# Kernel tuning notes

Measured on AMD Instinct MI355X. Metric: run time of the kernel, lower is better.

Reference implementation:

```python
import jax, jax.numpy as jnp
import numpy as np

B, N, F, C = 8, 1024, 2048, 4
H = F // 2

def setup_inputs() -> dict:
    key = jax.random.key(0)
    k0, k1, k2 = jax.random.split(key, 3)
    vectors = jax.random.normal(k0, (B, N, F), jnp.float32)  # pooled per-mask backbone features
    W1 = jax.random.normal(k1, (H, 2 * F), jnp.float32) * np.float32(1.0 / np.sqrt(2 * F))
    b1 = jnp.zeros((H,), jnp.float32)
    W2 = jax.random.normal(k2, (C, H), jnp.float32) * np.float32(1.0 / np.sqrt(H))
    b2 = jnp.zeros((C,), jnp.float32)
    return {"vectors": vectors, "W1": W1, "b1": b1, "W2": W2, "b2": b2}

def reference(vectors, W1, b1, W2, b2):
    # Original: for each pair (i, j): sigmoid(L2(L1(cat(v_i, v_j)))).
    # There is NO nonlinearity between the two Linears, so the composition is
    # exactly linear in (v_i, v_j):
    #   logits[b,i,j] = W2 @ (W1a v_i + W1b v_j + b1) + b2
    # which factors into two per-node projections + a pairwise broadcast add,
    # avoiding the [B,N,N,H] intermediate.
    f = vectors.shape[-1]
    W1a, W1b = W1[:, :f], W1[:, f:]
    p1 = jnp.einsum('bnh,ch->bnc', jnp.einsum('bnf,hf->bnh', vectors, W1a), W2)  # [B,N,C]
    p2 = jnp.einsum('bnh,ch->bnc', jnp.einsum('bnf,hf->bnh', vectors, W1b), W2)  # [B,N,C]
    const = W2 @ b1 + b2  # [C]
    logits = p1[:, :, None, :] + p2[:, None, :, :] + const  # [B, i, j, C]
    # torch code stacks j along dim=2 and i along dim=3 -> connections[b,c,j,i]
    connections = jax.nn.sigmoid(logits).transpose(0, 3, 2, 1)  # [B, C, N_j, N_i]
    return vectors, connections
```

## Files before the change

kernel.cpp:

```cpp
#include <hip/hip_runtime.h>
#include <hip/hip_bf16.h>

#define BB 8
#define NN 1024
#define FF 2048
#define CC 4
#define HH 1024
#define ROWS (BB * NN)
#define MELEMS (8 * FF)

typedef float f4 __attribute__((ext_vector_type(4)));

__device__ __forceinline__ float sigmoidf_fast(float x) {
    return __builtin_amdgcn_rcpf(1.0f + __expf(-x));
}

__device__ __forceinline__ float butterfly8(float a[8], int lane) {
    #pragma unroll
    for (int i = 0; i < 4; ++i) {
        float send = (lane & 1) ? a[i] : a[i + 4];
        float got = __shfl_xor(send, 1, 64);
        a[i] = ((lane & 1) ? a[i + 4] : a[i]) + got;
    }
    #pragma unroll
    for (int i = 0; i < 2; ++i) {
        float send = (lane & 2) ? a[i] : a[i + 2];
        float got = __shfl_xor(send, 2, 64);
        a[i] = ((lane & 2) ? a[i + 2] : a[i]) + got;
    }
    {
        float send = (lane & 4) ? a[0] : a[1];
        float got = __shfl_xor(send, 4, 64);
        a[0] = ((lane & 4) ? a[1] : a[0]) + got;
    }
    a[0] += __shfl_xor(a[0], 8, 64);
    a[0] += __shfl_xor(a[0], 16, 64);
    a[0] += __shfl_xor(a[0], 32, 64);
    return a[0];
}

__global__ __launch_bounds__(256) void k_fold(const float* __restrict__ W1,
                                              const float* __restrict__ W2,
                                              const float* __restrict__ b1,
                                              const float* __restrict__ b2,
                                              float* __restrict__ Mpart,
                                              float* __restrict__ cst,
                                              int hper, int nchunks) {
    int chunk = blockIdx.y;
    if (chunk == nchunks) {
        if (blockIdx.x != 0) return;
        int t = threadIdx.x;
        int c = t >> 6, lane = t & 63;
        float s = 0.f;
        for (int h = lane; h < HH; h += 64) s += W2[c * HH + h] * b1[h];
        #pragma unroll
        for (int off = 32; off; off >>= 1) s += __shfl_down(s, off);
        if (lane == 0) cst[c] = s + b2[c];
        return;
    }
    int k4 = (blockIdx.x * 256 + threadIdx.x) << 2;
    int half = k4 >> 11;
    int f = k4 & (FF - 1);
    int h0 = chunk * hper;
    f4 a0 = {0.f, 0.f, 0.f, 0.f}, a1 = a0, a2 = a0, a3 = a0;
    const float* base = W1 + (size_t)h0 * (2 * FF) + k4;
    #pragma unroll 16
    for (int i = 0; i < hper; ++i) {
        f4 wv = *(const f4*)(base + (size_t)i * (2 * FF));
        int h = h0 + i;
        float s0 = W2[0 * HH + h], s1 = W2[1 * HH + h];
        float s2 = W2[2 * HH + h], s3 = W2[3 * HH + h];
        a0 += wv * s0;
        a1 += wv * s1;
        a2 += wv * s2;
        a3 += wv * s3;
    }
    float* mp = Mpart + (size_t)chunk * MELEMS + (size_t)(half * 4) * FF + f;
    *(f4*)(mp + 0 * FF) = a0;
    *(f4*)(mp + 1 * FF) = a1;
    *(f4*)(mp + 2 * FF) = a2;
    *(f4*)(mp + 3 * FF) = a3;
}

__global__ __launch_bounds__(256) void k_reduce(const float* __restrict__ Mpart,
                                                float* __restrict__ M,
                                                int nchunks) {
    int idx4 = blockIdx.x * 256 + threadIdx.x;
    f4 s = {0.f, 0.f, 0.f, 0.f};
    const f4* mp = (const f4*)Mpart;
    #pragma unroll 16
    for (int p = 0; p < nchunks; ++p) s += mp[(size_t)p * (MELEMS / 4) + idx4];
    ((f4*)M)[idx4] = s;
}

__global__ __launch_bounds__(256) void k_pcompute(const float* __restrict__ v,
                                                  const float* __restrict__ M,
                                                  float* __restrict__ outv,
                                                  float* __restrict__ P1,
                                                  float* __restrict__ P2) {
    int t = threadIdx.x;
    int lane = t & 63, wvi = t >> 6;
    int f0 = t * 8;
    float w[8][8];
    #pragma unroll
    for (int j = 0; j < 8; ++j) {
        f4 a = *(const f4*)(M + j * FF + f0);
        f4 b = *(const f4*)(M + j * FF + f0 + 4);
        w[j][0] = a[0]; w[j][1] = a[1]; w[j][2] = a[2]; w[j][3] = a[3];
        w[j][4] = b[0]; w[j][5] = b[1]; w[j][6] = b[2]; w[j][7] = b[3];
    }
    int vidx = ((lane & 1) << 2) | (lane & 2) | ((lane >> 2) & 1);
    __shared__ float red[4][32];
    int row0 = blockIdx.x * 8;

    #pragma unroll
    for (int batch = 0; batch < 2; ++batch) {
        int rb = row0 + batch * 4;
        f4 va[4], vb[4];
        #pragma unroll
        for (int r = 0; r < 4; ++r) {
            const f4* vr = (const f4*)(v + (size_t)(rb + r) * FF + f0);
            va[r] = vr[0];
            vb[r] = vr[1];
        }
        #pragma unroll
        for (int r = 0; r < 4; ++r) {
            f4* po = (f4*)(outv + (size_t)(rb + r) * FF + f0);
            po[0] = va[r];
            po[1] = vb[r];
        }
        float fin[4];
        #pragma unroll
        for (int r = 0; r < 4; ++r) {
            float x[8] = {va[r][0], va[r][1], va[r][2], va[r][3],
                          vb[r][0], vb[r][1], vb[r][2], vb[r][3]};
            float acc[8];
            #pragma unroll
            for (int j = 0; j < 8; ++j) {
                float s = 0.f;
                #pragma unroll
                for (int k = 0; k < 8; ++k) s += x[k] * w[j][k];
                acc[j] = s;
            }
            fin[r] = butterfly8(acc, lane);
        }
        if (lane < 8) {
            #pragma unroll
            for (int r = 0; r < 4; ++r) red[r][wvi * 8 + vidx] = fin[r];
        }
        __syncthreads();
        if (t < 32) {
            int r = t >> 3, j = t & 7;
            float s = red[r][j] + red[r][8 + j] + red[r][16 + j] + red[r][24 + j];
            int row = rb + r;
            if (j < 4) P1[j * ROWS + row] = s;
            else       P2[(j - 4) * ROWS + row] = s;
        }
        __syncthreads();
    }
}

__global__ __launch_bounds__(256) void k_conn(const float* __restrict__ P1,
                                              const float* __restrict__ P2,
                                              const float* __restrict__ cst,
                                              float* __restrict__ out) {
    int t = threadIdx.x;
    #pragma unroll
    for (int it = 0; it < 4; ++it) {
        int r = blockIdx.x + it * 8192;
        int b = r >> 12;
        int c = (r >> 10) & 3;
        int j = r & (NN - 1);
        float s = P2[c * ROWS + b * NN + j] + cst[c];
        const f4* p1 = (const f4*)(P1 + c * ROWS + b * NN);
        f4 p = p1[t];
        f4 rs;
        rs[0] = sigmoidf_fast(p[0] + s);
        rs[1] = sigmoidf_fast(p[1] + s);
        rs[2] = sigmoidf_fast(p[2] + s);
        rs[3] = sigmoidf_fast(p[3] + s);
        *((f4*)(out + (size_t)r * NN) + t) = rs;
    }
}

extern "C" void kernel_launch(void* const* d_in, const int* in_sizes, int n_in,
                              void* d_out, int out_size, void* d_ws, size_t ws_size,
                              hipStream_t stream) {
    const float* vectors = (const float*)d_in[0];
    const float* W1 = (const float*)d_in[1];
    const float* b1 = (const float*)d_in[2];
    const float* W2 = (const float*)d_in[3];
    const float* b2 = (const float*)d_in[4];

    float* out_vectors = (float*)d_out;
    float* out_conn = (float*)d_out + (size_t)ROWS * FF;

    int nchunks = 16;
    {
        size_t fixed = (size_t)MELEMS + 16 + 2 * (size_t)CC * ROWS;
        if (ws_size >= ((size_t)128 * MELEMS + fixed) * sizeof(float)) nchunks = 128;
        else if (ws_size >= ((size_t)64 * MELEMS + fixed) * sizeof(float)) nchunks = 64;
        else if (ws_size >= ((size_t)32 * MELEMS + fixed) * sizeof(float)) nchunks = 32;
    }
    int hper = HH / nchunks;

    float* w = (float*)d_ws;
    float* Mpart = w;
    float* M     = Mpart + (size_t)nchunks * MELEMS;
    float* cst   = M + MELEMS;
    float* P1    = cst + 16;
    float* P2    = P1 + (size_t)CC * ROWS;

    k_fold<<<dim3(4, nchunks + 1), 256, 0, stream>>>(W1, W2, b1, b2, Mpart, cst, hper, nchunks);
    k_reduce<<<16, 256, 0, stream>>>(Mpart, M, nchunks);
    k_pcompute<<<ROWS / 8, 256, 0, stream>>>(vectors, M, out_vectors, P1, P2);
    k_conn<<<8192, 256, 0, stream>>>(P1, P2, cst, out_conn);
}
```

Measured before the change: 76.90 us.

## Fuse four kernels into one cooperative persistent kernel with grid syncs

Replaces the fold, reduce, per-node projection and pairwise sigmoid kernels with a single cooperative kernel of 512 blocks that runs the phases in order, separated by grid-wide barriers. Each later phase becomes a grid-stride loop. The aim is to remove the launch gaps and tail effects between kernels. The maximum chunk count drops from 128 to 64 so the fold phase fits inside the fixed grid. In exchange it adds three grid barriers, and the persistent grid may give lower occupancy and less latency hiding in the memory-bound phases.

```diff
diff --git a/kernel.cpp b/kernel.cpp
--- a/kernel.cpp
+++ b/kernel.cpp
@@ -1,5 +1,8 @@
 #include <hip/hip_runtime.h>
 #include <hip/hip_bf16.h>
+#include <hip/hip_cooperative_groups.h>
+
+namespace cg = cooperative_groups;
 
 #define BB 8
 #define NN 1024
@@ -8,6 +11,7 @@
 #define HH 1024
 #define ROWS (BB * NN)
 #define MELEMS (8 * FF)
+#define GRID 512
 
 typedef float f4 __attribute__((ext_vector_type(4)));
 
@@ -39,147 +43,147 @@
     return a[0];
 }
 
-__global__ __launch_bounds__(256) void k_fold(const float* __restrict__ W1,
+__global__ __launch_bounds__(256) void k_mega(const float* __restrict__ v,
+                                              const float* __restrict__ W1,
+                                              const float* __restrict__ b1,
                                               const float* __restrict__ W2,
-                                              const float* __restrict__ b1,
                                               const float* __restrict__ b2,
+                                              float* __restrict__ outv,
+                                              float* __restrict__ outc,
                                               float* __restrict__ Mpart,
+                                              float* __restrict__ M,
                                               float* __restrict__ cst,
+                                              float* __restrict__ P1,
+                                              float* __restrict__ P2,
                                               int hper, int nchunks) {
-    int chunk = blockIdx.y;
-    if (chunk == nchunks) {
-        if (blockIdx.x != 0) return;
-        int t = threadIdx.x;
-        int c = t >> 6, lane = t & 63;
-        float s = 0.f;
-        for (int h = lane; h < HH; h += 64) s += W2[c * HH + h] * b1[h];
-        #pragma unroll
-        for (int off = 32; off; off >>= 1) s += __shfl_down(s, off);
-        if (lane == 0) cst[c] = s + b2[c];
-        return;
-    }
-    int k4 = (blockIdx.x * 256 + threadIdx.x) << 2;
-    int half = k4 >> 11;
-    int f = k4 & (FF - 1);
-    int h0 = chunk * hper;
-    f4 a0 = {0.f, 0.f, 0.f, 0.f}, a1 = a0, a2 = a0, a3 = a0;
-    const float* base = W1 + (size_t)h0 * (2 * FF) + k4;
-    #pragma unroll 16
-    for (int i = 0; i < hper; ++i) {
-        f4 wv = *(const f4*)(base + (size_t)i * (2 * FF));
-        int h = h0 + i;
-        float s0 = W2[0 * HH + h], s1 = W2[1 * HH + h];
-        float s2 = W2[2 * HH + h], s3 = W2[3 * HH + h];
-        a0 += wv * s0;
-        a1 += wv * s1;
-        a2 += wv * s2;
-        a3 += wv * s3;
-    }
-    float* mp = Mpart + (size_t)chunk * MELEMS + (size_t)(half * 4) * FF + f;
-    *(f4*)(mp + 0 * FF) = a0;
-    *(f4*)(mp + 1 * FF) = a1;
-    *(f4*)(mp + 2 * FF) = a2;
-    *(f4*)(mp + 3 * FF) = a3;
-}
-
-__global__ __launch_bounds__(256) void k_reduce(const float* __restrict__ Mpart,
-                                                float* __restrict__ M,
-                                                int nchunks) {
-    int idx4 = blockIdx.x * 256 + threadIdx.x;
-    f4 s = {0.f, 0.f, 0.f, 0.f};
-    const f4* mp = (const f4*)Mpart;
-    #pragma unroll 16
-    for (int p = 0; p < nchunks; ++p) s += mp[(size_t)p * (MELEMS / 4) + idx4];
-    ((f4*)M)[idx4] = s;
-}
-
-__global__ __launch_bounds__(256) void k_pcompute(const float* __restrict__ v,
-                                                  const float* __restrict__ M,
-                                                  float* __restrict__ outv,
-                                                  float* __restrict__ P1,
-                                                  float* __restrict__ P2) {
+    cg::grid_group gridg = cg::this_grid();
+    int bid = blockIdx.x;
     int t = threadIdx.x;
     int lane = t & 63, wvi = t >> 6;
-    int f0 = t * 8;
-    float w[8][8];
-    #pragma unroll
-    for (int j = 0; j < 8; ++j) {
-        f4 a = *(const f4*)(M + j * FF + f0);
-        f4 b = *(const f4*)(M + j * FF + f0 + 4);
-        w[j][0] = a[0]; w[j][1] = a[1]; w[j][2] = a[2]; w[j][3] = a[3];
-        w[j][4] = b[0]; w[j][5] = b[1]; w[j][6] = b[2]; w[j][7] = b[3];
-    }
-    int vidx = ((lane & 1) << 2) | (lane & 2) | ((lane >> 2) & 1);
-    __shared__ float red[4][32];
-    int row0 = blockIdx.x * 8;
-
-    #pragma unroll
-    for (int batch = 0; batch < 2; ++batch) {
-        int rb = row0 + batch * 4;
-        f4 va[4], vb[4];
+
+    if (bid < nchunks * 4) {
+        int chunk = bid >> 2;
+        int k4 = ((bid & 3) * 256 + t) << 2;
+        int half = k4 >> 11;
+        int f = k4 & (FF - 1);
+        int h0 = chunk * hper;
+        f4 a0 = {0.f, 0.f, 0.f, 0.f}, a1 = a0, a2 = a0, a3 = a0;
+        const float* base = W1 + (size_t)h0 * (2 * FF) + k4;
+        #pragma unroll 16
+        for (int i = 0; i < hper; ++i) {
+            f4 wv = *(const f4*)(base + (size_t)i * (2 * FF));
+            int h = h0 + i;
+            float s0 = W2[0 * HH + h], s1 = W2[1 * HH + h];
+            float s2 = W2[2 * HH + h], s3 = W2[3 * HH + h];
+            a0 += wv * s0;
+            a1 += wv * s1;
+            a2 += wv * s2;
+            a3 += wv * s3;
+        }
+        float* mp = Mpart + (size_t)chunk * MELEMS + (size_t)(half * 4) * FF + f;
+        *(f4*)(mp + 0 * FF) = a0;
+        *(f4*)(mp + 1 * FF) = a1;
+        *(f4*)(mp + 2 * FF) = a2;
+        *(f4*)(mp + 3 * FF) = a3;
+    }
+    gridg.sync();
+
+    {
+        int gtid = bid * 256 + t;
+        if (gtid < MELEMS / 4) {
+            f4 s = {0.f, 0.f, 0.f, 0.f};
+            const f4* mp = (const f4*)Mpart;
+            #pragma unroll 16
+            for (int p = 0; p < nchunks; ++p) s += mp[(size_t)p * (MELEMS / 4) + gtid];
+            ((f4*)M)[gtid] = s;
+        }
+        if (bid == GRID - 1) {
+            int c = t >> 6;
+            float s = 0.f;
+            for (int h = lane; h < HH; h += 64) s += W2[c * HH + h] * b1[h];
+            #pragma unroll
+            for (int off = 32; off; off >>= 1) s += __shfl_down(s, off);
+            if (lane == 0) cst[c] = s + b2[c];
+        }
+    }
+    gridg.sync();
+
+    {
+        int f0 = t * 8;
+        float w[8][8];
         #pragma unroll
-        for (int r = 0; r < 4; ++r) {
-            const f4* vr = (const f4*)(v + (size_t)(rb + r) * FF + f0);
-            va[r] = vr[0];
-            vb[r] = vr[1];
-        }
-        #pragma unroll
-        for (int r = 0; r < 4; ++r) {
-            f4* po = (f4*)(outv + (size_t)(rb + r) * FF + f0);
-            po[0] = va[r];
-            po[1] = vb[r];
-        }
-        float fin[4];
-        #pragma unroll
-        for (int r = 0; r < 4; ++r) {
-            float x[8] = {va[r][0], va[r][1], va[r][2], va[r][3],
-                          vb[r][0], vb[r][1], vb[r][2], vb[r][3]};
-            float acc[8];
-            #pragma unroll
-            for (int j = 0; j < 8; ++j) {
-                float s = 0.f;
+        for (int j = 0; j < 8; ++j) {
+            f4 a = *(const f4*)(M + j * FF + f0);
+            f4 b = *(const f4*)(M + j * FF + f0 + 4);
+            w[j][0] = a[0]; w[j][1] = a[1]; w[j][2] = a[2]; w[j][3] = a[3];
+            w[j][4] = b[0]; w[j][5] = b[1]; w[j][6] = b[2]; w[j][7] = b[3];
+        }
+        int vidx = ((lane & 1) << 2) | (lane & 2) | ((lane >> 2) & 1);
+        __shared__ float red[4][32];
+        for (int u = bid; u < ROWS / 4; u += GRID) {
+            int rb = u * 4;
+            f4 va[4], vb[4];
+            #pragma unroll
+            for (int r = 0; r < 4; ++r) {
+                const f4* vr = (const f4*)(v + (size_t)(rb + r) * FF + f0);
+                va[r] = vr[0];
+                vb[r] = vr[1];
+            }
+            #pragma unroll
+            for (int r = 0; r < 4; ++r) {
+                f4* po = (f4*)(outv + (size_t)(rb + r) * FF + f0);
+                po[0] = va[r];
+                po[1] = vb[r];
+            }
+            float fin[4];
+            #pragma unroll
+            for (int r = 0; r < 4; ++r) {
+                float x[8] = {va[r][0], va[r][1], va[r][2], va[r][3],
+                              vb[r][0], vb[r][1], vb[r][2], vb[r][3]};
+                float acc[8];
                 #pragma unroll
-                for (int k = 0; k < 8; ++k) s += x[k] * w[j][k];
-                acc[j] = s;
-            }
-            fin[r] = butterfly8(acc, lane);
-        }
-        if (lane < 8) {
-            #pragma unroll
-            for (int r = 0; r < 4; ++r) red[r][wvi * 8 + vidx] = fin[r];
-        }
-        __syncthreads();
-        if (t < 32) {
-            int r = t >> 3, j = t & 7;
-            float s = red[r][j] + red[r][8 + j] + red[r][16 + j] + red[r][24 + j];
-            int row = rb + r;
-            if (j < 4) P1[j * ROWS + row] = s;
-            else       P2[(j - 4) * ROWS + row] = s;
-        }
-        __syncthreads();
-    }
-}
-
-__global__ __launch_bounds__(256) void k_conn(const float* __restrict__ P1,
-                                              const float* __restrict__ P2,
-                                              const float* __restrict__ cst,
-                                              float* __restrict__ out) {
-    int t = threadIdx.x;
-    #pragma unroll
-    for (int it = 0; it < 4; ++it) {
-        int r = blockIdx.x + it * 8192;
-        int b = r >> 12;
-        int c = (r >> 10) & 3;
-        int j = r & (NN - 1);
-        float s = P2[c * ROWS + b * NN + j] + cst[c];
-        const f4* p1 = (const f4*)(P1 + c * ROWS + b * NN);
-        f4 p = p1[t];
-        f4 rs;
-        rs[0] = sigmoidf_fast(p[0] + s);
-        rs[1] = sigmoidf_fast(p[1] + s);
-        rs[2] = sigmoidf_fast(p[2] + s);
-        rs[3] = sigmoidf_fast(p[3] + s);
-        *((f4*)(out + (size_t)r * NN) + t) = rs;
+                for (int j = 0; j < 8; ++j) {
+                    float s = 0.f;
+                    #pragma unroll
+                    for (int k = 0; k < 8; ++k) s += x[k] * w[j][k];
+                    acc[j] = s;
+                }
+                fin[r] = butterfly8(acc, lane);
+            }
+            if (lane < 8) {
+                #pragma unroll
+                for (int r = 0; r < 4; ++r) red[r][wvi * 8 + vidx] = fin[r];
+            }
+            __syncthreads();
+            if (t < 32) {
+                int r = t >> 3, j = t & 7;
+                float s = red[r][j] + red[r][8 + j] + red[r][16 + j] + red[r][24 + j];
+                int row = rb + r;
+                if (j < 4) P1[j * ROWS + row] = s;
+                else       P2[(j - 4) * ROWS + row] = s;
+            }
+            __syncthreads();
+        }
+    }
+    gridg.sync();
+
+    {
+        #pragma unroll 4
+        for (int it = 0; it < 64; ++it) {
+            int r = bid + it * GRID;
+            int b = r >> 12;
+            int c = (r >> 10) & 3;
+            int j = r & (NN - 1);
+            float s = P2[c * ROWS + b * NN + j] + cst[c];
+            const f4* p1 = (const f4*)(P1 + c * ROWS + b * NN);
+            f4 p = p1[t];
+            f4 rs;
+            rs[0] = sigmoidf_fast(p[0] + s);
+            rs[1] = sigmoidf_fast(p[1] + s);
+            rs[2] = sigmoidf_fast(p[2] + s);
+            rs[3] = sigmoidf_fast(p[3] + s);
+            *((f4*)(outc + (size_t)r * NN) + t) = rs;
+        }
     }
 }
 
@@ -198,8 +202,7 @@
     int nchunks = 16;
     {
         size_t fixed = (size_t)MELEMS + 16 + 2 * (size_t)CC * ROWS;
-        if (ws_size >= ((size_t)128 * MELEMS + fixed) * sizeof(float)) nchunks = 128;
-        else if (ws_size >= ((size_t)64 * MELEMS + fixed) * sizeof(float)) nchunks = 64;
+        if (ws_size >= ((size_t)64 * MELEMS + fixed) * sizeof(float)) nchunks = 64;
         else if (ws_size >= ((size_t)32 * MELEMS + fixed) * sizeof(float)) nchunks = 32;
     }
     int hper = HH / nchunks;
@@ -211,8 +214,12 @@
     float* P1    = cst + 16;
     float* P2    = P1 + (size_t)CC * ROWS;
 
-    k_fold<<<dim3(4, nchunks + 1), 256, 0, stream>>>(W1, W2, b1, b2, Mpart, cst, hper, nchunks);
-    k_reduce<<<16, 256, 0, stream>>>(Mpart, M, nchunks);
-    k_pcompute<<<ROWS / 8, 256, 0, stream>>>(vectors, M, out_vectors, P1, P2);
-    k_conn<<<8192, 256, 0, stream>>>(P1, P2, cst, out_conn);
-}
+    void* args[] = {
+        (void*)&vectors, (void*)&W1, (void*)&b1, (void*)&W2, (void*)&b2,
+        (void*)&out_vectors, (void*)&out_conn,
+        (void*)&Mpart, (void*)&M, (void*)&cst, (void*)&P1, (void*)&P2,
+        (void*)&hper, (void*)&nchunks
+    };
+    hipLaunchCooperativeKernel((const void*)k_mega, dim3(GRID), dim3(256),
+                               args, 0, stream);
+}
```

Result: slower. 234.8 us (+205.3%).
